# Kernel optimization log

Hardware: AMD Instinct MI355X
Metric: run time of the kernel (lower is better)

Reference implementation:

```python
import jax, jax.numpy as jnp
import numpy as np

C = 1024          # columns
K = 16            # cells per column
S = 32            # distal segments per cell
Y = 128           # synapses per segment
N = C * K         # num cells
PERM_THR = 0.5
ACT_THR = 10
LR = 0.1          # volatile learning rate
MOD = 1.0         # modulation_signal


def setup_inputs() -> dict:
    key = jax.random.key(0)
    k1, k2, k3, k4, k5 = jax.random.split(key, 5)
    x = jax.random.uniform(k1, (C,)) < 0.03                      # sparse column SDR
    prev_active_cells = jax.random.uniform(k2, (N,)) < 0.12      # prev-step active cells
    distal_connections = jax.random.randint(k3, (N, S, Y), 0, N, dtype=jnp.int32)
    volatile_permanences = jax.random.uniform(k4, (N, S, Y), dtype=jnp.float32)
    consolidated_permanences = jax.random.uniform(k5, (N, S, Y), dtype=jnp.float32) * 0.6
    return {
        "x": x,
        "prev_active_cells": prev_active_cells,
        "distal_connections": distal_connections,
        "volatile_permanences": volatile_permanences,
        "consolidated_permanences": consolidated_permanences,
    }


def reference(x, prev_active_cells, distal_connections, volatile_permanences, consolidated_permanences):
    conn = jnp.clip(distal_connections, 0, N - 1)                # [N,S,Y]
    x_active = x.astype(bool)                                    # [C]
    prev_any = prev_active_cells.any()

    # ---- phase 1: predictive state per column from prev_active_cells ----
    presyn_prev = prev_active_cells[conn]                        # [N,S,Y] irregular gather
    connected = (volatile_permanences > PERM_THR) | (consolidated_permanences > PERM_THR)
    active_syn = (connected & presyn_prev).sum(-1)               # [N,S]
    pred_cell = (active_syn >= ACT_THR).any(-1)                  # [N]
    pred_col = pred_cell.reshape(C, K)                           # [C,K]
    col_predicted = pred_col.any(-1)                             # [C]

    # ---- burst winner selection (unthresholded overlaps, argmax over K*S) ----
    overlaps = presyn_prev.sum(-1).astype(jnp.int32)             # [N,S]
    best_flat = jnp.argmax(overlaps.reshape(C, K * S), axis=-1)  # [C]
    burst_winner_local = best_flat // S                          # [C] (== 0 when no prev activity, matching torch fallback)
    burst_winner_mask = jax.nn.one_hot(burst_winner_local, K, dtype=bool)  # [C,K]

    winner = jnp.where(col_predicted[:, None], pred_col, burst_winner_mask)  # [C,K]
    winner = winner & x_active[:, None]                          # only active columns

    # new active cells: only bursting columns set cells (predicted columns set none, per source)
    new_active = jnp.broadcast_to((x_active & ~col_predicted)[:, None], (C, K))
    new_active_flat = new_active.reshape(-1)                     # [N]

    # ---- learning: update volatile permanences on each winner cell's best segment ----
    best_seg = jnp.argmax(overlaps, axis=-1)                     # [N]
    rows = jnp.arange(N)
    presyn_best = presyn_prev[rows, best_seg]                    # [N,Y]
    old_row = volatile_permanences[rows, best_seg]               # [N,Y]
    pot = LR * MOD
    pun = pot * 0.1
    new_row = jnp.clip(old_row + jnp.where(presyn_best, pot, -pun), 0.0, 1.0)
    learn_mask = winner.reshape(-1) & prev_any                   # [N] (torch skips learning if no prev activity)
    vol_new = volatile_permanences.at[rows, best_seg].set(
        jnp.where(learn_mask[:, None], new_row, old_row))

    # ---- phase 2: predictive state for next step from new active cells + updated perms ----
    presyn_new = new_active_flat[conn]                           # [N,S,Y]
    connected2 = (vol_new > PERM_THR) | (consolidated_permanences > PERM_THR)
    pred_next = (((connected2 & presyn_new).sum(-1)) >= ACT_THR).any(-1)  # [N]

    num_active = x_active.sum()
    num_pred = (x_active & col_predicted).sum()
    acc = jnp.where(num_active > 0,
                    num_pred.astype(jnp.float32) / jnp.maximum(num_active, 1).astype(jnp.float32),
                    jnp.float32(1.0))
    return new_active_flat, pred_next, acc
```

## Files before the change

kernel.cpp:

```cpp
#include <hip/hip_runtime.h>
#include <stdint.h>

#define C_ 1024
#define K_ 16
#define S_ 32
#define Y_ 128
#define N_ (C_ * K_)
#define ACT_THR 10
#define PERM_THR 0.5f
#define POT 0.1f
#define PUN 0.01f

typedef float f4 __attribute__((ext_vector_type(4)));
typedef int   i4 __attribute__((ext_vector_type(4)));

#define WS_NUM_ACTIVE 0
#define WS_NUM_PRED   1
#define WS_NBURST     2
#define WS_LEARN_CNT  3
#define WS_PREV_ANY   4
#define WS_BURSTMASK  8
#define WS_PREVMASK   64
#define WS_CELLINFO   1024
#define WS_LIST       (1024 + N_)
#define WS_CONBITS    65536


__global__ __launch_bounds__(512) void pack_kernel(const int* __restrict__ prev,
                                                   unsigned* __restrict__ ws) {
    const int tid = threadIdx.x;
    if (tid < 64) ws[tid] = 0u;
    __syncthreads();
    const int4* p = reinterpret_cast<const int4*>(prev + tid * 32);
    unsigned m = 0u;
    #pragma unroll
    for (int q = 0; q < 8; ++q) {
        const int4 v = p[q];
        m |= (v.x != 0 ? 1u : 0u) << (q * 4 + 0);
        m |= (v.y != 0 ? 1u : 0u) << (q * 4 + 1);
        m |= (v.z != 0 ? 1u : 0u) << (q * 4 + 2);
        m |= (v.w != 0 ? 1u : 0u) << (q * 4 + 3);
    }
    ws[WS_PREVMASK + tid] = m;
    const bool any = (__ballot(m != 0u) != 0ull);
    if ((tid & 63) == 0 && any) atomicOr(&ws[WS_PREV_ANY], 1u);
}

__global__ __launch_bounds__(256) void phase1c_kernel(const int*   __restrict__ conn,
                                                      const float* __restrict__ vol,
                                                      const float* __restrict__ cons,
                                                      unsigned long long* __restrict__ conbits,
                                                      unsigned*    __restrict__ ws) {
    __shared__ unsigned prevmask[512];
    const int tid = threadIdx.x;
    for (int i = tid; i < 512; i += 256) prevmask[i] = ws[WS_PREVMASK + i];
    __syncthreads();

    const int wave = tid >> 6;
    const int lane = tid & 63;
    const int half = lane >> 5;
    const int l32  = lane & 31;
    const int sh   = half * 32;

    const int cellA = blockIdx.x * 8 + wave;
    const int cellB = cellA + 4;
    const size_t baseA = (size_t)cellA * (S_ * Y_) + (size_t)half * Y_ + (size_t)(l32 * 4);
    const size_t baseB = (size_t)cellB * (S_ * Y_) + (size_t)half * Y_ + (size_t)(l32 * 4);

    auto proc = [&](const i4 cv, const f4 vv, const f4 sv, const int i,
                    unsigned& key, bool& predf, unsigned long long& bits) {
        const unsigned nib = ((vv[0] > PERM_THR || sv[0] > PERM_THR) ? 1u : 0u)
                           | ((vv[1] > PERM_THR || sv[1] > PERM_THR) ? 2u : 0u)
                           | ((vv[2] > PERM_THR || sv[2] > PERM_THR) ? 4u : 0u)
                           | ((vv[3] > PERM_THR || sv[3] > PERM_THR) ? 8u : 0u);
        bits |= ((unsigned long long)nib) << (4 * i);

        const int m0 = min(max(cv[0], 0), N_ - 1);
        const int m1 = min(max(cv[1], 0), N_ - 1);
        const int m2 = min(max(cv[2], 0), N_ - 1);
        const int m3 = min(max(cv[3], 0), N_ - 1);
        const bool p0 = (prevmask[m0 >> 5] >> (m0 & 31)) & 1u;
        const bool p1 = (prevmask[m1 >> 5] >> (m1 & 31)) & 1u;
        const bool p2 = (prevmask[m2 >> 5] >> (m2 & 31)) & 1u;
        const bool p3 = (prevmask[m3 >> 5] >> (m3 & 31)) & 1u;

        const uint64_t bp0 = __ballot(p0), bp1 = __ballot(p1),
                       bp2 = __ballot(p2), bp3 = __ballot(p3);
        const uint64_t ba0 = __ballot(p0 && (nib & 1u)), ba1 = __ballot(p1 && (nib & 2u)),
                       ba2 = __ballot(p2 && (nib & 4u)), ba3 = __ballot(p3 && (nib & 8u));

        const int ov = __popc((unsigned)(bp0 >> sh)) + __popc((unsigned)(bp1 >> sh)) +
                       __popc((unsigned)(bp2 >> sh)) + __popc((unsigned)(bp3 >> sh));
        const int ac = __popc((unsigned)(ba0 >> sh)) + __popc((unsigned)(ba1 >> sh)) +
                       __popc((unsigned)(ba2 >> sh)) + __popc((unsigned)(ba3 >> sh));

        predf |= (ac >= ACT_THR);
        const int seg = 2 * i + half;
        const unsigned k2 = ((unsigned)ov << 6) | (unsigned)(63 - seg);
        key = max(key, k2);
    };

    i4 cA = *reinterpret_cast<const i4*>(conn + baseA);
    i4 cB = *reinterpret_cast<const i4*>(conn + baseB);
    f4 vA = __builtin_nontemporal_load(reinterpret_cast<const f4*>(vol  + baseA));
    f4 vB = __builtin_nontemporal_load(reinterpret_cast<const f4*>(vol  + baseB));
    f4 sA = __builtin_nontemporal_load(reinterpret_cast<const f4*>(cons + baseA));
    f4 sB = __builtin_nontemporal_load(reinterpret_cast<const f4*>(cons + baseB));

    unsigned keyA = 0u, keyB = 0u;
    bool pfA = false, pfB = false;
    unsigned long long bitsA = 0ull, bitsB = 0ull;

    #pragma unroll 3
    for (int i = 0; i < 15; ++i) {
        const size_t nA = baseA + (size_t)(i + 1) * 256;
        const size_t nB = baseB + (size_t)(i + 1) * 256;
        const i4 cA1 = *reinterpret_cast<const i4*>(conn + nA);
        const i4 cB1 = *reinterpret_cast<const i4*>(conn + nB);
        const f4 vA1 = __builtin_nontemporal_load(reinterpret_cast<const f4*>(vol  + nA));
        const f4 vB1 = __builtin_nontemporal_load(reinterpret_cast<const f4*>(vol  + nB));
        const f4 sA1 = __builtin_nontemporal_load(reinterpret_cast<const f4*>(cons + nA));
        const f4 sB1 = __builtin_nontemporal_load(reinterpret_cast<const f4*>(cons + nB));

        proc(cA, vA, sA, i, keyA, pfA, bitsA);
        proc(cB, vB, sB, i, keyB, pfB, bitsB);

        cA = cA1; vA = vA1; sA = sA1;
        cB = cB1; vB = vB1; sB = sB1;
    }
    proc(cA, vA, sA, 15, keyA, pfA, bitsA);
    proc(cB, vB, sB, 15, keyB, pfB, bitsB);

    const unsigned fkA = max(keyA, (unsigned)__shfl_xor((int)keyA, 32));
    const unsigned fkB = max(keyB, (unsigned)__shfl_xor((int)keyB, 32));
    const bool fpA = (__any(pfA ? 1 : 0) != 0);
    const bool fpB = (__any(pfB ? 1 : 0) != 0);
    if (lane == 0) {
        ws[WS_CELLINFO + cellA] = (fpA ? 1u : 0u) | ((unsigned)(63 - (fkA & 63u)) << 8) | ((fkA >> 6) << 16);
        ws[WS_CELLINFO + cellB] = (fpB ? 1u : 0u) | ((unsigned)(63 - (fkB & 63u)) << 8) | ((fkB >> 6) << 16);
    }
    conbits[(size_t)cellA * 64 + lane] = bitsA;
    conbits[(size_t)cellB * 64 + lane] = bitsB;
}

__global__ __launch_bounds__(256) void column_kernel(const int* __restrict__ x,
                                                     unsigned*  __restrict__ ws,
                                                     float*     __restrict__ out_new_active) {
    const int c = blockIdx.x * 256 + threadIdx.x;
    if (c >= C_) return;
    const bool xa = (x[c] != 0);
    const int base = c * K_;

    unsigned info[K_];
    bool colpred = false;
    int bo = -1, bk = 0;
    #pragma unroll
    for (int k = 0; k < K_; ++k) {
        const unsigned inf = ws[WS_CELLINFO + base + k];
        info[k] = inf;
        if (inf & 1u) colpred = true;
        const int ov = (int)((inf >> 16) & 0xFFu);
        if (ov > bo) { bo = ov; bk = k; }
    }

    const bool burst = xa && !colpred;
    const float nav = burst ? 1.0f : 0.0f;
    #pragma unroll
    for (int k = 0; k < K_; ++k) out_new_active[base + k] = nav;

    if (xa) {
        atomicAdd(&ws[WS_NUM_ACTIVE], 1u);
        if (colpred) atomicAdd(&ws[WS_NUM_PRED], 1u);
    }
    if (burst) {
        atomicAdd(&ws[WS_NBURST], 1u);
        atomicOr(&ws[WS_BURSTMASK + (c >> 5)], 1u << (c & 31));
    }
    if (xa) {
        if (colpred) {
            #pragma unroll
            for (int k = 0; k < K_; ++k) {
                if (info[k] & 1u) {
                    const unsigned i = atomicAdd(&ws[WS_LEARN_CNT], 1u);
                    ws[WS_LIST + i] = (unsigned)(base + k);
                }
            }
        } else {
            const unsigned i = atomicAdd(&ws[WS_LEARN_CNT], 1u);
            ws[WS_LIST + i] = (unsigned)(base + bk);
        }
    }
}

__global__ __launch_bounds__(256) void learnb_kernel(const int*   __restrict__ conn,
                                                     float*       __restrict__ vol,
                                                     const float* __restrict__ cons,
                                                     unsigned*    __restrict__ ws,
                                                     float*       __restrict__ out_acc) {
    __shared__ unsigned prevmask[512];
    const int tid = threadIdx.x;
    for (int i = tid; i < 512; i += 256) prevmask[i] = ws[WS_PREVMASK + i];
    __syncthreads();

    if (blockIdx.x == 0 && tid == 0) {
        const int na  = (int)ws[WS_NUM_ACTIVE];
        const int np_ = (int)ws[WS_NUM_PRED];
        out_acc[0] = (na > 0) ? ((float)np_ / (float)na) : 1.0f;
    }
    if (ws[WS_PREV_ANY] == 0u) return;

    const int cnt = (int)ws[WS_LEARN_CNT];
    const int hw  = (blockIdx.x * 256 + tid) >> 5;
    const int g   = tid & 31;
    const int nhw = gridDim.x * 8;
    unsigned* conbits32 = ws + WS_CONBITS;

    for (int e = hw; e < cnt; e += nhw) {
        const int cellv = (int)ws[WS_LIST + e];
        const int seg   = (int)((ws[WS_CELLINFO + cellv] >> 8) & 0xFFu);
        const size_t base = ((size_t)cellv * S_ + seg) * Y_ + (size_t)(g * 4);
        const int4   cv = *reinterpret_cast<const int4*>(conn + base);
        float4       vv = *reinterpret_cast<float4*>(vol + base);
        const float4 sv = *reinterpret_cast<const float4*>(cons + base);
        const int m0 = min(max(cv.x, 0), N_ - 1);
        const int m1 = min(max(cv.y, 0), N_ - 1);
        const int m2 = min(max(cv.z, 0), N_ - 1);
        const int m3 = min(max(cv.w, 0), N_ - 1);
        const bool p0 = (prevmask[m0 >> 5] >> (m0 & 31)) & 1u;
        const bool p1 = (prevmask[m1 >> 5] >> (m1 & 31)) & 1u;
        const bool p2 = (prevmask[m2 >> 5] >> (m2 & 31)) & 1u;
        const bool p3 = (prevmask[m3 >> 5] >> (m3 & 31)) & 1u;
        vv.x = fminf(fmaxf(vv.x + (p0 ? POT : -PUN), 0.0f), 1.0f);
        vv.y = fminf(fmaxf(vv.y + (p1 ? POT : -PUN), 0.0f), 1.0f);
        vv.z = fminf(fmaxf(vv.z + (p2 ? POT : -PUN), 0.0f), 1.0f);
        vv.w = fminf(fmaxf(vv.w + (p3 ? POT : -PUN), 0.0f), 1.0f);
        *reinterpret_cast<float4*>(vol + base) = vv;

        const unsigned nib = ((vv.x > PERM_THR || sv.x > PERM_THR) ? 1u : 0u)
                           | ((vv.y > PERM_THR || sv.y > PERM_THR) ? 2u : 0u)
                           | ((vv.z > PERM_THR || sv.z > PERM_THR) ? 4u : 0u)
                           | ((vv.w > PERM_THR || sv.w > PERM_THR) ? 8u : 0u);
        const int chunk = seg >> 1;
        const int slot  = (seg & 1) * 32 + g;
        const unsigned idx = (unsigned)(cellv * 128 + slot * 2 + (chunk >> 3));
        const int shn = 4 * (chunk & 7);
        const unsigned old = conbits32[idx];
        conbits32[idx] = (old & ~(0xFu << shn)) | (nib << shn);
    }
}

__global__ __launch_bounds__(256) void phase2c_kernel(const int* __restrict__ conn,
                                                      const unsigned long long* __restrict__ conbits,
                                                      const unsigned* __restrict__ ws,
                                                      float* __restrict__ out_pred_next) {
    __shared__ unsigned nburst_s;
    __shared__ unsigned burstmask[32];
    const int tid = threadIdx.x;
    if (tid == 0) nburst_s = ws[WS_NBURST];
    if (tid >= 64 && tid < 96) burstmask[tid - 64] = ws[WS_BURSTMASK + (tid - 64)];
    __syncthreads();

    const int cbase = ((int)gridDim.x - 1 - (int)blockIdx.x) * 16;
    if (nburst_s == 0u) {
        if (tid < 16) out_pred_next[cbase + tid] = 0.0f;
        return;
    }

    const int wave = tid >> 6;
    const int lane = tid & 63;
    const int half = lane >> 5;
    const int l32  = lane & 31;
    const int sh   = half * 32;

    const int c0i = cbase + wave;
    const size_t off = (size_t)half * Y_ + (size_t)(l32 * 4);
    const size_t b0 = (size_t)(c0i     ) * (S_ * Y_) + off;
    const size_t b1 = (size_t)(c0i + 4 ) * (S_ * Y_) + off;
    const size_t b2 = (size_t)(c0i + 8 ) * (S_ * Y_) + off;
    const size_t b3 = (size_t)(c0i + 12) * (S_ * Y_) + off;

    unsigned long long q0 = conbits[(size_t)(c0i     ) * 64 + lane];
    unsigned long long q1 = conbits[(size_t)(c0i + 4 ) * 64 + lane];
    unsigned long long q2 = conbits[(size_t)(c0i + 8 ) * 64 + lane];
    unsigned long long q3 = conbits[(size_t)(c0i + 12) * 64 + lane];

    auto proc = [&](const i4 cv, const unsigned nib, bool& predf) {
        const int m0 = min(max(cv[0], 0), N_ - 1) >> 4;
        const int m1 = min(max(cv[1], 0), N_ - 1) >> 4;
        const int m2 = min(max(cv[2], 0), N_ - 1) >> 4;
        const int m3 = min(max(cv[3], 0), N_ - 1) >> 4;
        const bool p0 = (burstmask[m0 >> 5] >> (m0 & 31)) & 1u;
        const bool p1 = (burstmask[m1 >> 5] >> (m1 & 31)) & 1u;
        const bool p2 = (burstmask[m2 >> 5] >> (m2 & 31)) & 1u;
        const bool p3 = (burstmask[m3 >> 5] >> (m3 & 31)) & 1u;
        const uint64_t ba0 = __ballot(p0 && (nib & 1u)), ba1 = __ballot(p1 && (nib & 2u)),
                       ba2 = __ballot(p2 && (nib & 4u)), ba3 = __ballot(p3 && (nib & 8u));
        const int ac = __popc((unsigned)(ba0 >> sh)) + __popc((unsigned)(ba1 >> sh)) +
                       __popc((unsigned)(ba2 >> sh)) + __popc((unsigned)(ba3 >> sh));
        predf |= (ac >= ACT_THR);
    };

    i4 a0 = *reinterpret_cast<const i4*>(conn + b0);
    i4 a1 = *reinterpret_cast<const i4*>(conn + b1);
    i4 a2 = *reinterpret_cast<const i4*>(conn + b2);
    i4 a3 = *reinterpret_cast<const i4*>(conn + b3);

    bool f0 = false, f1 = false, f2 = false, f3 = false;

    #pragma unroll 3
    for (int i = 0; i < 15; ++i) {
        const size_t d = (size_t)(i + 1) * 256;
        const i4 n0 = *reinterpret_cast<const i4*>(conn + b0 + d);
        const i4 n1 = *reinterpret_cast<const i4*>(conn + b1 + d);
        const i4 n2 = *reinterpret_cast<const i4*>(conn + b2 + d);
        const i4 n3 = *reinterpret_cast<const i4*>(conn + b3 + d);

        proc(a0, (unsigned)q0 & 0xFu, f0); q0 >>= 4;
        proc(a1, (unsigned)q1 & 0xFu, f1); q1 >>= 4;
        proc(a2, (unsigned)q2 & 0xFu, f2); q2 >>= 4;
        proc(a3, (unsigned)q3 & 0xFu, f3); q3 >>= 4;

        a0 = n0; a1 = n1; a2 = n2; a3 = n3;
    }
    proc(a0, (unsigned)q0 & 0xFu, f0);
    proc(a1, (unsigned)q1 & 0xFu, f1);
    proc(a2, (unsigned)q2 & 0xFu, f2);
    proc(a3, (unsigned)q3 & 0xFu, f3);

    const bool g0 = (__any(f0 ? 1 : 0) != 0);
    const bool g1 = (__any(f1 ? 1 : 0) != 0);
    const bool g2 = (__any(f2 ? 1 : 0) != 0);
    const bool g3 = (__any(f3 ? 1 : 0) != 0);
    if (lane == 0) {
        out_pred_next[c0i     ] = g0 ? 1.0f : 0.0f;
        out_pred_next[c0i + 4 ] = g1 ? 1.0f : 0.0f;
        out_pred_next[c0i + 8 ] = g2 ? 1.0f : 0.0f;
        out_pred_next[c0i + 12] = g3 ? 1.0f : 0.0f;
    }
}

__global__ __launch_bounds__(256) void phase1_old(const int*   __restrict__ conn,
                                                  const float* __restrict__ vol,
                                                  const float* __restrict__ cons,
                                                  unsigned*    __restrict__ ws) {
    __shared__ unsigned prevmask[512];
    const int tid = threadIdx.x;
    for (int i = tid; i < 512; i += 256) prevmask[i] = ws[WS_PREVMASK + i];
    __syncthreads();

    const int wave = tid >> 6;
    const int lane = tid & 63;
    const int half = lane >> 5;
    const int l32  = lane & 31;
    const int sh   = half * 32;

    #pragma unroll 1
    for (int ci = 0; ci < 2; ++ci) {
        const int cell = blockIdx.x * 8 + wave + ci * 4;
        const size_t cellbase = (size_t)cell * (S_ * Y_) + (size_t)(l32 * 4);

        size_t a = cellbase + (size_t)half * Y_;
        int4   cv_n = *reinterpret_cast<const int4*>(conn + a);
        float4 vv_n = *reinterpret_cast<const float4*>(vol + a);
        float4 sv_n = *reinterpret_cast<const float4*>(cons + a);

        unsigned key = 0u;
        bool predf = false;

        #pragma unroll 2
        for (int i = 0; i < 16; ++i) {
            const int4   cv = cv_n;
            const float4 vv = vv_n;
            const float4 sv = sv_n;
            if (i < 15) {
                const size_t nb = cellbase + (size_t)(2 * (i + 1) + half) * Y_;
                cv_n = *reinterpret_cast<const int4*>(conn + nb);
                vv_n = *reinterpret_cast<const float4*>(vol + nb);
                sv_n = *reinterpret_cast<const float4*>(cons + nb);
            }

            const int m0 = min(max(cv.x, 0), N_ - 1);
            const int m1 = min(max(cv.y, 0), N_ - 1);
            const int m2 = min(max(cv.z, 0), N_ - 1);
            const int m3 = min(max(cv.w, 0), N_ - 1);
            const bool p0 = (prevmask[m0 >> 5] >> (m0 & 31)) & 1u;
            const bool p1 = (prevmask[m1 >> 5] >> (m1 & 31)) & 1u;
            const bool p2 = (prevmask[m2 >> 5] >> (m2 & 31)) & 1u;
            const bool p3 = (prevmask[m3 >> 5] >> (m3 & 31)) & 1u;
            const bool c0 = (vv.x > PERM_THR) || (sv.x > PERM_THR);
            const bool c1 = (vv.y > PERM_THR) || (sv.y > PERM_THR);
            const bool c2 = (vv.z > PERM_THR) || (sv.z > PERM_THR);
            const bool c3 = (vv.w > PERM_THR) || (sv.w > PERM_THR);

            const uint64_t bp0 = __ballot(p0), bp1 = __ballot(p1),
                           bp2 = __ballot(p2), bp3 = __ballot(p3);
            const uint64_t ba0 = __ballot(p0 && c0), ba1 = __ballot(p1 && c1),
                           ba2 = __ballot(p2 && c2), ba3 = __ballot(p3 && c3);

            const int ov = __popc((unsigned)(bp0 >> sh)) + __popc((unsigned)(bp1 >> sh)) +
                           __popc((unsigned)(bp2 >> sh)) + __popc((unsigned)(bp3 >> sh));
            const int ac = __popc((unsigned)(ba0 >> sh)) + __popc((unsigned)(ba1 >> sh)) +
                           __popc((unsigned)(ba2 >> sh)) + __popc((unsigned)(ba3 >> sh));

            predf |= (ac >= ACT_THR);
            const int seg = 2 * i + half;
            const unsigned k2 = ((unsigned)ov << 6) | (unsigned)(63 - seg);
            key = max(key, k2);
        }

        const unsigned okey = (unsigned)__shfl_xor((int)key, 32);
        const unsigned fkey = max(key, okey);
        const bool fpred = (__any(predf ? 1 : 0) != 0);
        if (lane == 0) {
            const int bo = (int)(fkey >> 6);
            const int bs = 63 - (int)(fkey & 63u);
            ws[WS_CELLINFO + cell] = (fpred ? 1u : 0u) | ((unsigned)bs << 8) | ((unsigned)bo << 16);
        }
    }
}

__global__ __launch_bounds__(256) void learn_old(const int* __restrict__ conn,
                                                 float*     __restrict__ vol,
                                                 unsigned*  __restrict__ ws,
                                                 float*     __restrict__ out_acc) {
    __shared__ unsigned prevmask[512];
    const int tid = threadIdx.x;
    for (int i = tid; i < 512; i += 256) prevmask[i] = ws[WS_PREVMASK + i];
    __syncthreads();

    if (blockIdx.x == 0 && tid == 0) {
        const int na  = (int)ws[WS_NUM_ACTIVE];
        const int np_ = (int)ws[WS_NUM_PRED];
        out_acc[0] = (na > 0) ? ((float)np_ / (float)na) : 1.0f;
    }
    if (ws[WS_PREV_ANY] == 0u) return;

    const int cnt    = (int)ws[WS_LEARN_CNT];
    const int wave   = (blockIdx.x * 256 + tid) >> 6;
    const int lane   = tid & 63;
    const int nwaves = gridDim.x * 4;

    for (int e = wave; e < cnt; e += nwaves) {
        const int cell = (int)ws[WS_LIST + e];
        const int seg  = (int)((ws[WS_CELLINFO + cell] >> 8) & 0xFFu);
        const size_t base = ((size_t)cell * S_ + seg) * Y_ + (size_t)(lane * 2);
        const int2 cv = *reinterpret_cast<const int2*>(conn + base);
        float2 vv = *reinterpret_cast<const float2*>(vol + base);
        const int m0 = min(max(cv.x, 0), N_ - 1);
        const int m1 = min(max(cv.y, 0), N_ - 1);
        const bool p0 = (prevmask[m0 >> 5] >> (m0 & 31)) & 1u;
        const bool p1 = (prevmask[m1 >> 5] >> (m1 & 31)) & 1u;
        vv.x = fminf(fmaxf(vv.x + (p0 ? POT : -PUN), 0.0f), 1.0f);
        vv.y = fminf(fmaxf(vv.y + (p1 ? POT : -PUN), 0.0f), 1.0f);
        *reinterpret_cast<float2*>(vol + base) = vv;
    }
}

__global__ __launch_bounds__(256) void phase2_old(const int*   __restrict__ conn,
                                                  const float* __restrict__ vol,
                                                  const float* __restrict__ cons,
                                                  const unsigned* __restrict__ ws,
                                                  float* __restrict__ out_pred_next) {
    __shared__ unsigned nburst_s;
    __shared__ unsigned burstmask[32];
    const int tid = threadIdx.x;
    if (tid == 0) nburst_s = ws[WS_NBURST];
    if (tid >= 64 && tid < 96) burstmask[tid - 64] = ws[WS_BURSTMASK + (tid - 64)];
    __syncthreads();

    const int cbase = blockIdx.x * 8;
    if (nburst_s == 0u) {
        if (tid < 8) out_pred_next[cbase + tid] = 0.0f;
        return;
    }

    const int wave = tid >> 6;
    const int lane = tid & 63;
    const int half = lane >> 5;
    const int l32  = lane & 31;
    const int sh   = half * 32;

    #pragma unroll 1
    for (int ci = 0; ci < 2; ++ci) {
        const int cell = cbase + wave + ci * 4;
        const size_t cellbase = (size_t)cell * (S_ * Y_) + (size_t)(l32 * 4);

        size_t a = cellbase + (size_t)half * Y_;
        int4   cv_n = *reinterpret_cast<const int4*>(conn + a);
        float4 vv_n = *reinterpret_cast<const float4*>(vol + a);
        float4 sv_n = *reinterpret_cast<const float4*>(cons + a);

        bool predf = false;

        #pragma unroll 2
        for (int i = 0; i < 16; ++i) {
            const int4   cv = cv_n;
            const float4 vv = vv_n;
            const float4 sv = sv_n;
            if (i < 15) {
                const size_t nb = cellbase + (size_t)(2 * (i + 1) + half) * Y_;
                cv_n = *reinterpret_cast<const int4*>(conn + nb);
                vv_n = *reinterpret_cast<const float4*>(vol + nb);
                sv_n = *reinterpret_cast<const float4*>(cons + nb);
            }

            const int m0 = min(max(cv.x, 0), N_ - 1) >> 4;
            const int m1 = min(max(cv.y, 0), N_ - 1) >> 4;
            const int m2 = min(max(cv.z, 0), N_ - 1) >> 4;
            const int m3 = min(max(cv.w, 0), N_ - 1) >> 4;
            const bool p0 = (burstmask[m0 >> 5] >> (m0 & 31)) & 1u;
            const bool p1 = (burstmask[m1 >> 5] >> (m1 & 31)) & 1u;
            const bool p2 = (burstmask[m2 >> 5] >> (m2 & 31)) & 1u;
            const bool p3 = (burstmask[m3 >> 5] >> (m3 & 31)) & 1u;
            const bool c0 = (vv.x > PERM_THR) || (sv.x > PERM_THR);
            const bool c1 = (vv.y > PERM_THR) || (sv.y > PERM_THR);
            const bool c2 = (vv.z > PERM_THR) || (sv.z > PERM_THR);
            const bool c3 = (vv.w > PERM_THR) || (sv.w > PERM_THR);

            const uint64_t ba0 = __ballot(p0 && c0), ba1 = __ballot(p1 && c1),
                           ba2 = __ballot(p2 && c2), ba3 = __ballot(p3 && c3);
            const int ac = __popc((unsigned)(ba0 >> sh)) + __popc((unsigned)(ba1 >> sh)) +
                           __popc((unsigned)(ba2 >> sh)) + __popc((unsigned)(ba3 >> sh));
            predf |= (ac >= ACT_THR);
        }

        const bool fpred = (__any(predf ? 1 : 0) != 0);
        if (lane == 0) out_pred_next[cell] = fpred ? 1.0f : 0.0f;
    }
}

extern "C" void kernel_launch(void* const* d_in, const int* in_sizes, int n_in,
                              void* d_out, int out_size, void* d_ws, size_t ws_size,
                              hipStream_t stream) {
    const int*   x    = (const int*)d_in[0];
    const int*   prev = (const int*)d_in[1];
    const int*   conn = (const int*)d_in[2];
    float*       vol  = (float*)d_in[3];
    const float* cons = (const float*)d_in[4];
    float*    out = (float*)d_out;
    unsigned* ws  = (unsigned*)d_ws;

    const size_t need = (size_t)WS_CONBITS * 4 + (size_t)N_ * 64 * 8;

    pack_kernel<<<1, 512, 0, stream>>>(prev, ws);

    if (ws_size >= need) {
        unsigned long long* conbits = (unsigned long long*)(ws + WS_CONBITS);
        phase1c_kernel<<<N_ / 8,  256, 0, stream>>>(conn, vol, cons, conbits, ws);
        column_kernel <<<C_ / 256, 256, 0, stream>>>(x, ws, out);
        learnb_kernel <<<64,      256, 0, stream>>>(conn, vol, cons, ws, out + 2 * N_);
        phase2c_kernel<<<N_ / 16, 256, 0, stream>>>(conn, conbits, ws, out + N_);
    } else {
        phase1_old<<<2048, 256, 0, stream>>>(conn, vol, cons, ws);
        column_kernel<<<C_ / 256, 256, 0, stream>>>(x, ws, out);
        learn_old<<<64, 256, 0, stream>>>(conn, vol, ws, out + 2 * N_);
        phase2_old<<<2048, 256, 0, stream>>>(conn, vol, cons, ws, out + N_);
    }
}
```

Before: 667.5 us.

## Pack column index and connected bit into 16-bit array for phase 2

```diff
diff --git a/kernel.cpp b/kernel.cpp
--- a/kernel.cpp
+++ b/kernel.cpp
@@ -13,6 +13,7 @@
 
 typedef float f4 __attribute__((ext_vector_type(4)));
 typedef int   i4 __attribute__((ext_vector_type(4)));
+typedef unsigned short u16x8 __attribute__((ext_vector_type(8)));
 
 #define WS_NUM_ACTIVE 0
 #define WS_NUM_PRED   1
@@ -23,7 +24,7 @@
 #define WS_PREVMASK   64
 #define WS_CELLINFO   1024
 #define WS_LIST       (1024 + N_)
-#define WS_CONBITS    65536
+#define WS_PACKED_B   (256 * 1024)
 
 
 __global__ __launch_bounds__(512) void pack_kernel(const int* __restrict__ prev,
@@ -46,11 +47,11 @@
     if ((tid & 63) == 0 && any) atomicOr(&ws[WS_PREV_ANY], 1u);
 }
 
-__global__ __launch_bounds__(256) void phase1c_kernel(const int*   __restrict__ conn,
-                                                      const float* __restrict__ vol,
-                                                      const float* __restrict__ cons,
-                                                      unsigned long long* __restrict__ conbits,
-                                                      unsigned*    __restrict__ ws) {
+__global__ __launch_bounds__(256, 4) void phase1c_kernel(const int*   __restrict__ conn,
+                                                         const float* __restrict__ vol,
+                                                         const float* __restrict__ cons,
+                                                         unsigned short* __restrict__ packed,
+                                                         unsigned*    __restrict__ ws) {
     __shared__ unsigned prevmask[512];
     const int tid = threadIdx.x;
     for (int i = tid; i < 512; i += 256) prevmask[i] = ws[WS_PREVMASK + i];
@@ -68,17 +69,24 @@
     const size_t baseB = (size_t)cellB * (S_ * Y_) + (size_t)half * Y_ + (size_t)(l32 * 4);
 
     auto proc = [&](const i4 cv, const f4 vv, const f4 sv, const int i,
-                    unsigned& key, bool& predf, unsigned long long& bits) {
+                    const size_t pbase, unsigned& key, bool& predf) {
         const unsigned nib = ((vv[0] > PERM_THR || sv[0] > PERM_THR) ? 1u : 0u)
                            | ((vv[1] > PERM_THR || sv[1] > PERM_THR) ? 2u : 0u)
                            | ((vv[2] > PERM_THR || sv[2] > PERM_THR) ? 4u : 0u)
                            | ((vv[3] > PERM_THR || sv[3] > PERM_THR) ? 8u : 0u);
-        bits |= ((unsigned long long)nib) << (4 * i);
 
         const int m0 = min(max(cv[0], 0), N_ - 1);
         const int m1 = min(max(cv[1], 0), N_ - 1);
         const int m2 = min(max(cv[2], 0), N_ - 1);
         const int m3 = min(max(cv[3], 0), N_ - 1);
+
+        ushort4 pk;
+        pk.x = (unsigned short)((m0 >> 4) | ((nib & 1u) ? 0x8000u : 0u));
+        pk.y = (unsigned short)((m1 >> 4) | ((nib & 2u) ? 0x8000u : 0u));
+        pk.z = (unsigned short)((m2 >> 4) | ((nib & 4u) ? 0x8000u : 0u));
+        pk.w = (unsigned short)((m3 >> 4) | ((nib & 8u) ? 0x8000u : 0u));
+        *reinterpret_cast<ushort4*>(packed + pbase + (size_t)i * 256) = pk;
+
         const bool p0 = (prevmask[m0 >> 5] >> (m0 & 31)) & 1u;
         const bool p1 = (prevmask[m1 >> 5] >> (m1 & 31)) & 1u;
         const bool p2 = (prevmask[m2 >> 5] >> (m2 & 31)) & 1u;
@@ -100,8 +108,8 @@
         key = max(key, k2);
     };
 
-    i4 cA = *reinterpret_cast<const i4*>(conn + baseA);
-    i4 cB = *reinterpret_cast<const i4*>(conn + baseB);
+    i4 cA = __builtin_nontemporal_load(reinterpret_cast<const i4*>(conn + baseA));
+    i4 cB = __builtin_nontemporal_load(reinterpret_cast<const i4*>(conn + baseB));
     f4 vA = __builtin_nontemporal_load(reinterpret_cast<const f4*>(vol  + baseA));
     f4 vB = __builtin_nontemporal_load(reinterpret_cast<const f4*>(vol  + baseB));
     f4 sA = __builtin_nontemporal_load(reinterpret_cast<const f4*>(cons + baseA));
@@ -109,27 +117,26 @@
 
     unsigned keyA = 0u, keyB = 0u;
     bool pfA = false, pfB = false;
-    unsigned long long bitsA = 0ull, bitsB = 0ull;
 
     #pragma unroll 3
     for (int i = 0; i < 15; ++i) {
         const size_t nA = baseA + (size_t)(i + 1) * 256;
         const size_t nB = baseB + (size_t)(i + 1) * 256;
-        const i4 cA1 = *reinterpret_cast<const i4*>(conn + nA);
-        const i4 cB1 = *reinterpret_cast<const i4*>(conn + nB);
+        const i4 cA1 = __builtin_nontemporal_load(reinterpret_cast<const i4*>(conn + nA));
+        const i4 cB1 = __builtin_nontemporal_load(reinterpret_cast<const i4*>(conn + nB));
         const f4 vA1 = __builtin_nontemporal_load(reinterpret_cast<const f4*>(vol  + nA));
         const f4 vB1 = __builtin_nontemporal_load(reinterpret_cast<const f4*>(vol  + nB));
         const f4 sA1 = __builtin_nontemporal_load(reinterpret_cast<const f4*>(cons + nA));
         const f4 sB1 = __builtin_nontemporal_load(reinterpret_cast<const f4*>(cons + nB));
 
-        proc(cA, vA, sA, i, keyA, pfA, bitsA);
-        proc(cB, vB, sB, i, keyB, pfB, bitsB);
+        proc(cA, vA, sA, i, baseA, keyA, pfA);
+        proc(cB, vB, sB, i, baseB, keyB, pfB);
 
         cA = cA1; vA = vA1; sA = sA1;
         cB = cB1; vB = vB1; sB = sB1;
     }
-    proc(cA, vA, sA, 15, keyA, pfA, bitsA);
-    proc(cB, vB, sB, 15, keyB, pfB, bitsB);
+    proc(cA, vA, sA, 15, baseA, keyA, pfA);
+    proc(cB, vB, sB, 15, baseB, keyB, pfB);
 
     const unsigned fkA = max(keyA, (unsigned)__shfl_xor((int)keyA, 32));
     const unsigned fkB = max(keyB, (unsigned)__shfl_xor((int)keyB, 32));
@@ -139,8 +146,6 @@
         ws[WS_CELLINFO + cellA] = (fpA ? 1u : 0u) | ((unsigned)(63 - (fkA & 63u)) << 8) | ((fkA >> 6) << 16);
         ws[WS_CELLINFO + cellB] = (fpB ? 1u : 0u) | ((unsigned)(63 - (fkB & 63u)) << 8) | ((fkB >> 6) << 16);
     }
-    conbits[(size_t)cellA * 64 + lane] = bitsA;
-    conbits[(size_t)cellB * 64 + lane] = bitsB;
 }
 
 __global__ __launch_bounds__(256) void column_kernel(const int* __restrict__ x,
@@ -195,6 +200,7 @@
 __global__ __launch_bounds__(256) void learnb_kernel(const int*   __restrict__ conn,
                                                      float*       __restrict__ vol,
                                                      const float* __restrict__ cons,
+                                                     unsigned short* __restrict__ packed,
                                                      unsigned*    __restrict__ ws,
                                                      float*       __restrict__ out_acc) {
     __shared__ unsigned prevmask[512];
@@ -213,7 +219,6 @@
     const int hw  = (blockIdx.x * 256 + tid) >> 5;
     const int g   = tid & 31;
     const int nhw = gridDim.x * 8;
-    unsigned* conbits32 = ws + WS_CONBITS;
 
     for (int e = hw; e < cnt; e += nhw) {
         const int cellv = (int)ws[WS_LIST + e];
@@ -236,23 +241,18 @@
         vv.w = fminf(fmaxf(vv.w + (p3 ? POT : -PUN), 0.0f), 1.0f);
         *reinterpret_cast<float4*>(vol + base) = vv;
 
-        const unsigned nib = ((vv.x > PERM_THR || sv.x > PERM_THR) ? 1u : 0u)
-                           | ((vv.y > PERM_THR || sv.y > PERM_THR) ? 2u : 0u)
-                           | ((vv.z > PERM_THR || sv.z > PERM_THR) ? 4u : 0u)
-                           | ((vv.w > PERM_THR || sv.w > PERM_THR) ? 8u : 0u);
-        const int chunk = seg >> 1;
-        const int slot  = (seg & 1) * 32 + g;
-        const unsigned idx = (unsigned)(cellv * 128 + slot * 2 + (chunk >> 3));
-        const int shn = 4 * (chunk & 7);
-        const unsigned old = conbits32[idx];
-        conbits32[idx] = (old & ~(0xFu << shn)) | (nib << shn);
-    }
-}
-
-__global__ __launch_bounds__(256) void phase2c_kernel(const int* __restrict__ conn,
-                                                      const unsigned long long* __restrict__ conbits,
-                                                      const unsigned* __restrict__ ws,
-                                                      float* __restrict__ out_pred_next) {
+        ushort4 pk;
+        pk.x = (unsigned short)((m0 >> 4) | ((vv.x > PERM_THR || sv.x > PERM_THR) ? 0x8000u : 0u));
+        pk.y = (unsigned short)((m1 >> 4) | ((vv.y > PERM_THR || sv.y > PERM_THR) ? 0x8000u : 0u));
+        pk.z = (unsigned short)((m2 >> 4) | ((vv.z > PERM_THR || sv.z > PERM_THR) ? 0x8000u : 0u));
+        pk.w = (unsigned short)((m3 >> 4) | ((vv.w > PERM_THR || sv.w > PERM_THR) ? 0x8000u : 0u));
+        *reinterpret_cast<ushort4*>(packed + base) = pk;
+    }
+}
+
+__global__ __launch_bounds__(256, 4) void phase2d_kernel(const unsigned short* __restrict__ packed,
+                                                         const unsigned* __restrict__ ws,
+                                                         float* __restrict__ out_pred_next) {
     __shared__ unsigned nburst_s;
     __shared__ unsigned burstmask[32];
     const int tid = threadIdx.x;
@@ -268,64 +268,57 @@
 
     const int wave = tid >> 6;
     const int lane = tid & 63;
-    const int half = lane >> 5;
-    const int l32  = lane & 31;
-    const int sh   = half * 32;
 
     const int c0i = cbase + wave;
-    const size_t off = (size_t)half * Y_ + (size_t)(l32 * 4);
+    const size_t off = (size_t)(lane * 8);
     const size_t b0 = (size_t)(c0i     ) * (S_ * Y_) + off;
     const size_t b1 = (size_t)(c0i + 4 ) * (S_ * Y_) + off;
     const size_t b2 = (size_t)(c0i + 8 ) * (S_ * Y_) + off;
     const size_t b3 = (size_t)(c0i + 12) * (S_ * Y_) + off;
 
-    unsigned long long q0 = conbits[(size_t)(c0i     ) * 64 + lane];
-    unsigned long long q1 = conbits[(size_t)(c0i + 4 ) * 64 + lane];
-    unsigned long long q2 = conbits[(size_t)(c0i + 8 ) * 64 + lane];
-    unsigned long long q3 = conbits[(size_t)(c0i + 12) * 64 + lane];
-
-    auto proc = [&](const i4 cv, const unsigned nib, bool& predf) {
-        const int m0 = min(max(cv[0], 0), N_ - 1) >> 4;
-        const int m1 = min(max(cv[1], 0), N_ - 1) >> 4;
-        const int m2 = min(max(cv[2], 0), N_ - 1) >> 4;
-        const int m3 = min(max(cv[3], 0), N_ - 1) >> 4;
-        const bool p0 = (burstmask[m0 >> 5] >> (m0 & 31)) & 1u;
-        const bool p1 = (burstmask[m1 >> 5] >> (m1 & 31)) & 1u;
-        const bool p2 = (burstmask[m2 >> 5] >> (m2 & 31)) & 1u;
-        const bool p3 = (burstmask[m3 >> 5] >> (m3 & 31)) & 1u;
-        const uint64_t ba0 = __ballot(p0 && (nib & 1u)), ba1 = __ballot(p1 && (nib & 2u)),
-                       ba2 = __ballot(p2 && (nib & 4u)), ba3 = __ballot(p3 && (nib & 8u));
-        const int ac = __popc((unsigned)(ba0 >> sh)) + __popc((unsigned)(ba1 >> sh)) +
-                       __popc((unsigned)(ba2 >> sh)) + __popc((unsigned)(ba3 >> sh));
-        predf |= (ac >= ACT_THR);
+    auto proc = [&](const u16x8 pv, bool& predf) {
+        int cnt = 0;
+        #pragma unroll
+        for (int e = 0; e < 8; ++e) {
+            const unsigned val = (unsigned)pv[e];
+            const unsigned col = val & 1023u;
+            const unsigned con = val >> 15;
+            const unsigned b = (burstmask[col >> 5] >> (col & 31)) & 1u;
+            cnt += (int)(con & b);
+        }
+        cnt += __shfl_xor(cnt, 1);
+        cnt += __shfl_xor(cnt, 2);
+        cnt += __shfl_xor(cnt, 4);
+        cnt += __shfl_xor(cnt, 8);
+        predf |= (cnt >= ACT_THR);
     };
 
-    i4 a0 = *reinterpret_cast<const i4*>(conn + b0);
-    i4 a1 = *reinterpret_cast<const i4*>(conn + b1);
-    i4 a2 = *reinterpret_cast<const i4*>(conn + b2);
-    i4 a3 = *reinterpret_cast<const i4*>(conn + b3);
+    u16x8 a0 = *reinterpret_cast<const u16x8*>(packed + b0);
+    u16x8 a1 = *reinterpret_cast<const u16x8*>(packed + b1);
+    u16x8 a2 = *reinterpret_cast<const u16x8*>(packed + b2);
+    u16x8 a3 = *reinterpret_cast<const u16x8*>(packed + b3);
 
     bool f0 = false, f1 = false, f2 = false, f3 = false;
 
-    #pragma unroll 3
-    for (int i = 0; i < 15; ++i) {
-        const size_t d = (size_t)(i + 1) * 256;
-        const i4 n0 = *reinterpret_cast<const i4*>(conn + b0 + d);
-        const i4 n1 = *reinterpret_cast<const i4*>(conn + b1 + d);
-        const i4 n2 = *reinterpret_cast<const i4*>(conn + b2 + d);
-        const i4 n3 = *reinterpret_cast<const i4*>(conn + b3 + d);
-
-        proc(a0, (unsigned)q0 & 0xFu, f0); q0 >>= 4;
-        proc(a1, (unsigned)q1 & 0xFu, f1); q1 >>= 4;
-        proc(a2, (unsigned)q2 & 0xFu, f2); q2 >>= 4;
-        proc(a3, (unsigned)q3 & 0xFu, f3); q3 >>= 4;
+    #pragma unroll 2
+    for (int j = 0; j < 7; ++j) {
+        const size_t d = (size_t)(j + 1) * 512;
+        const u16x8 n0 = *reinterpret_cast<const u16x8*>(packed + b0 + d);
+        const u16x8 n1 = *reinterpret_cast<const u16x8*>(packed + b1 + d);
+        const u16x8 n2 = *reinterpret_cast<const u16x8*>(packed + b2 + d);
+        const u16x8 n3 = *reinterpret_cast<const u16x8*>(packed + b3 + d);
+
+        proc(a0, f0);
+        proc(a1, f1);
+        proc(a2, f2);
+        proc(a3, f3);
 
         a0 = n0; a1 = n1; a2 = n2; a3 = n3;
     }
-    proc(a0, (unsigned)q0 & 0xFu, f0);
-    proc(a1, (unsigned)q1 & 0xFu, f1);
-    proc(a2, (unsigned)q2 & 0xFu, f2);
-    proc(a3, (unsigned)q3 & 0xFu, f3);
+    proc(a0, f0);
+    proc(a1, f1);
+    proc(a2, f2);
+    proc(a3, f3);
 
     const bool g0 = (__any(f0 ? 1 : 0) != 0);
     const bool g1 = (__any(f1 ? 1 : 0) != 0);
@@ -540,16 +533,16 @@
     float*    out = (float*)d_out;
     unsigned* ws  = (unsigned*)d_ws;
 
-    const size_t need = (size_t)WS_CONBITS * 4 + (size_t)N_ * 64 * 8;
+    const size_t need = (size_t)WS_PACKED_B + (size_t)N_ * S_ * Y_ * 2;
 
     pack_kernel<<<1, 512, 0, stream>>>(prev, ws);
 
     if (ws_size >= need) {
-        unsigned long long* conbits = (unsigned long long*)(ws + WS_CONBITS);
-        phase1c_kernel<<<N_ / 8,  256, 0, stream>>>(conn, vol, cons, conbits, ws);
+        unsigned short* packed = (unsigned short*)((char*)d_ws + WS_PACKED_B);
+        phase1c_kernel<<<N_ / 8,  256, 0, stream>>>(conn, vol, cons, packed, ws);
         column_kernel <<<C_ / 256, 256, 0, stream>>>(x, ws, out);
-        learnb_kernel <<<64,      256, 0, stream>>>(conn, vol, cons, ws, out + 2 * N_);
-        phase2c_kernel<<<N_ / 16, 256, 0, stream>>>(conn, conbits, ws, out + N_);
+        learnb_kernel <<<64,      256, 0, stream>>>(conn, vol, cons, packed, ws, out + 2 * N_);
+        phase2d_kernel<<<N_ / 16, 256, 0, stream>>>(packed, ws, out + N_);
     } else {
         phase1_old<<<2048, 256, 0, stream>>>(conn, vol, cons, ws);
         column_kernel<<<C_ / 256, 256, 0, stream>>>(x, ws, out);
```

Result: slower. 691.2 us (+3.6%).
